# Kernel optimization log

Measured on AMD Instinct MI355X. Metric: run time of the kernel, lower is better.

Reference implementation:

```python
import jax, jax.numpy as jnp
import numpy as np

B, L = 16, 2048
D_MODEL, D_INNER, D_STATE, DT_RANK, D_CONV = 128, 256, 16, 8, 4
N_LAYERS, N_CLASSES = 4, 5
EPS = 1e-5


def setup_inputs() -> dict:
    key = jax.random.key(0)
    ks = jax.random.split(key, 12)
    rn = lambda k, shape, s=0.02: jax.random.normal(k, shape, jnp.float32) * s
    A_log = jnp.log(jnp.arange(1, D_STATE + 1, dtype=jnp.float32))  # S4D-real init
    return dict(
        x=jax.random.normal(ks[0], (B, L, 12), jnp.float32),
        enc_w=rn(ks[1], (D_MODEL, 12), 0.1),
        enc_b=jnp.zeros((D_MODEL,), jnp.float32),
        norm_w=jnp.ones((N_LAYERS, D_MODEL), jnp.float32),
        in_proj_w=rn(ks[2], (N_LAYERS, 2 * D_INNER, D_MODEL)),
        conv_w=rn(ks[3], (N_LAYERS, D_INNER, D_CONV), 0.1),
        conv_b=jnp.zeros((N_LAYERS, D_INNER), jnp.float32),
        x_proj_w=rn(ks[4], (N_LAYERS, DT_RANK + 2 * D_STATE, D_INNER)),
        dt_proj_w=rn(ks[5], (N_LAYERS, D_INNER, DT_RANK), 0.1),
        dt_proj_b=rn(ks[6], (N_LAYERS, D_INNER), 0.1),
        A_log=jnp.broadcast_to(A_log, (N_LAYERS, D_INNER, D_STATE)) + 0.0,
        Dp=jnp.ones((N_LAYERS, D_INNER), jnp.float32),
        out_proj_w=rn(ks[7], (N_LAYERS, D_MODEL, D_INNER)),
        norm_f_w=jnp.ones((D_MODEL,), jnp.float32),
        cls_w=rn(ks[8], (N_CLASSES, D_MODEL), 0.05),
        cls_b=jnp.zeros((N_CLASSES,), jnp.float32),
    )


def rmsnorm(x, w):
    return x * jax.lax.rsqrt(jnp.mean(x * x, axis=-1, keepdims=True) + EPS) * w


def causal_depthwise_conv(x, w, b):
    # x: [b, l, di]; w: [di, k]; causal (left) padding, groups=di
    xc = x.transpose(0, 2, 1)  # [b, di, l]
    y = jax.lax.conv_general_dilated(
        xc, w[:, None, :], window_strides=(1,), padding=[(D_CONV - 1, 0)],
        dimension_numbers=("NCH", "OIH", "NCH"), feature_group_count=D_INNER)
    return (y + b[None, :, None]).transpose(0, 2, 1)


def selective_scan(u, delta, A, Bm, Cm, Dv):
    # u, delta: [b,l,di]; A: [di,n]; Bm, Cm: [b,l,n]; Dv: [di]
    dA = jnp.exp(jnp.einsum("bld,dn->bldn", delta, A))          # [b,l,di,n]
    dBu = jnp.einsum("bld,bln,bld->bldn", delta, Bm, u)          # [b,l,di,n]

    def step(h, inp):
        dA_t, dBu_t, C_t = inp
        h = dA_t * h + dBu_t                                     # [b,di,n]
        y = jnp.einsum("bdn,bn->bd", h, C_t)
        return h, y

    h0 = jnp.zeros((u.shape[0], u.shape[2], A.shape[1]), u.dtype)
    xs = (dA.transpose(1, 0, 2, 3), dBu.transpose(1, 0, 2, 3), Cm.transpose(1, 0, 2))
    _, ys = jax.lax.scan(step, h0, xs)
    return ys.transpose(1, 0, 2) + u * Dv


def mamba_block(x, in_w, cw, cb, xp_w, dt_w, dt_b, A_log_i, D_i, out_w):
    xz = jnp.einsum("bld,ed->ble", x, in_w)                      # [b,l,2*di]
    xm, z = xz[..., :D_INNER], xz[..., D_INNER:]
    xm = jax.nn.silu(causal_depthwise_conv(xm, cw, cb))
    x_dbl = jnp.einsum("bld,ed->ble", xm, xp_w)                  # [b,l,dt_rank+2n]
    dt = x_dbl[..., :DT_RANK]
    Bm = x_dbl[..., DT_RANK:DT_RANK + D_STATE]
    Cm = x_dbl[..., DT_RANK + D_STATE:]
    delta = jax.nn.softplus(jnp.einsum("blr,dr->bld", dt, dt_w) + dt_b)
    A = -jnp.exp(A_log_i)
    y = selective_scan(xm, delta, A, Bm, Cm, D_i)
    y = y * jax.nn.silu(z)
    return jnp.einsum("bld,ed->ble", y, out_w)


def reference(x, enc_w, enc_b, norm_w, in_proj_w, conv_w, conv_b, x_proj_w,
              dt_proj_w, dt_proj_b, A_log, Dp, out_proj_w, norm_f_w, cls_w, cls_b):
    h = jnp.einsum("blc,dc->bld", x, enc_w) + enc_b               # conv1d k=1 encoder
    for i in range(N_LAYERS):
        h = mamba_block(rmsnorm(h, norm_w[i]), in_proj_w[i], conv_w[i], conv_b[i],
                        x_proj_w[i], dt_proj_w[i], dt_proj_b[i], A_log[i], Dp[i],
                        out_proj_w[i]) + h
    h = rmsnorm(h, norm_f_w)
    pooled = jnp.mean(h, axis=1)                                  # AdaptiveAvgPool1d(1)
    return pooled @ cls_w.T + cls_b                               # [B, n_classes]
```

## Files before the change

### kernel.cpp

```cpp
#include <hip/hip_runtime.h>
#include <hip/hip_bf16.h>
#include <cstddef>

#define BB 16
#define LL 2048
#define DM 128
#define DI 256
#define DS 16
#define MP (BB*LL)
#define NSEG 64
#define SEGLEN (LL/NSEG)
#define YSTR 264
#define XSTR 40

typedef __attribute__((ext_vector_type(8))) short bf16x8;
typedef __attribute__((ext_vector_type(4))) short bf16x4s;
typedef __attribute__((ext_vector_type(8))) unsigned int ux8;
typedef __attribute__((ext_vector_type(4))) float f32x4;
typedef __hip_bfloat16 bf16;
typedef unsigned int uint;

__device__ inline void bf16split(float x, bf16& h, bf16& l) {
  h = __float2bfloat16(x);
  l = __float2bfloat16(x - __bfloat162float(h));
}
__device__ inline float bf2f(bf16 v) { return __bfloat162float(v); }
__device__ inline void split_bits2(float x, short& hs, short& ls) {
  bf16 hb = __float2bfloat16(x);
  bf16 lb = __float2bfloat16(x - __bfloat162float(hb));
  hs = *(short*)&hb;
  ls = *(short*)&lb;
}
__device__ inline short bfbits(float x) {
  bf16 b = __float2bfloat16(x);
  return *(short*)&b;
}
__device__ inline float sigm(float x) {
  return __builtin_amdgcn_rcpf(1.f + __expf(-x));
}
__device__ inline uint pk2(short h, short l) {
  return (uint)(unsigned short)h | ((uint)(unsigned short)l << 16);
}
__device__ inline uint pack_hl(float x) {
  short hs, ls; split_bits2(x, hs, ls);
  return pk2(hs, ls);
}
__device__ inline float unpack_hl(uint w) {
  return __uint_as_float(w << 16) + __uint_as_float(w & 0xffff0000u);
}

__global__ __launch_bounds__(256, 2) void gemm_inproj_conv(
    const bf16* __restrict__ Ah, const bf16* __restrict__ Al,
    const bf16* __restrict__ Wh, const bf16* __restrict__ Wl,
    const bf16* __restrict__ Xh, const bf16* __restrict__ Xl,
    const float* __restrict__ cw, const float* __restrict__ cb,
    uint* __restrict__ zs_pk, uint* __restrict__ u_pk,
    float* __restrict__ C) {
  __shared__ uint  xmb[35 * 260];
  __shared__ short ubh[32 * 264];
  __shared__ short ubl[32 * 264];
  __shared__ float scw[DI * 4 + DI];
  int tid = threadIdx.x;
  {
    float4 w4 = *(const float4*)(cw + tid * 4);
    *(float4*)(scw + tid * 4) = w4;
    scw[DI * 4 + tid] = cb[tid];
  }
  int wave = tid >> 6, lane = tid & 63;
  int r16 = lane & 15, quad = lane >> 4;
  int m0 = blockIdx.x * 32;

  size_t arow[3];
#pragma unroll
  for (int rt = 0; rt < 3; rt++) {
    int rg = m0 - 16 + rt * 16 + r16;
    if (rg < 0) rg = 0;
    arow[rt] = (size_t)rg * DM + quad * 8;
  }
  size_t browx[4], browz[4];
#pragma unroll
  for (int ct = 0; ct < 4; ct++) {
    browx[ct] = (size_t)(wave * 64 + ct * 16 + r16) * DM + quad * 8;
    browz[ct] = (size_t)(256 + wave * 64 + ct * 16 + r16) * DM + quad * 8;
  }
  f32x4 accx[3][4] = {};
  f32x4 accz[2][4] = {};
#pragma unroll
  for (int kk = 0; kk < 4; kk++) {
    int ko = kk * 32;
    bf16x8 ah[3], al[3], bxh[4], bxl[4], bzh[4], bzl[4];
#pragma unroll
    for (int rt = 0; rt < 3; rt++) {
      ah[rt] = *(const bf16x8*)(Ah + arow[rt] + ko);
      al[rt] = *(const bf16x8*)(Al + arow[rt] + ko);
    }
#pragma unroll
    for (int ct = 0; ct < 4; ct++) {
      bxh[ct] = *(const bf16x8*)(Wh + browx[ct] + ko);
      bxl[ct] = *(const bf16x8*)(Wl + browx[ct] + ko);
      bzh[ct] = *(const bf16x8*)(Wh + browz[ct] + ko);
      bzl[ct] = *(const bf16x8*)(Wl + browz[ct] + ko);
    }
#pragma unroll
    for (int rt = 0; rt < 3; rt++)
#pragma unroll
      for (int ct = 0; ct < 4; ct++) {
        accx[rt][ct] = __builtin_amdgcn_mfma_f32_16x16x32_bf16(ah[rt], bxh[ct], accx[rt][ct], 0, 0, 0);
        accx[rt][ct] = __builtin_amdgcn_mfma_f32_16x16x32_bf16(ah[rt], bxl[ct], accx[rt][ct], 0, 0, 0);
        accx[rt][ct] = __builtin_amdgcn_mfma_f32_16x16x32_bf16(al[rt], bxh[ct], accx[rt][ct], 0, 0, 0);
      }
#pragma unroll
    for (int rz = 0; rz < 2; rz++)
#pragma unroll
      for (int ct = 0; ct < 4; ct++) {
        accz[rz][ct] = __builtin_amdgcn_mfma_f32_16x16x32_bf16(ah[rz + 1], bzh[ct], accz[rz][ct], 0, 0, 0);
        accz[rz][ct] = __builtin_amdgcn_mfma_f32_16x16x32_bf16(ah[rz + 1], bzl[ct], accz[rz][ct], 0, 0, 0);
        accz[rz][ct] = __builtin_amdgcn_mfma_f32_16x16x32_bf16(al[rz + 1], bzh[ct], accz[rz][ct], 0, 0, 0);
      }
  }
#pragma unroll
  for (int rz = 0; rz < 2; rz++)
#pragma unroll
    for (int ct = 0; ct < 4; ct++)
#pragma unroll
      for (int r = 0; r < 4; r++) {
        int row = m0 + rz * 16 + quad * 4 + r;
        int col = wave * 64 + ct * 16 + r16;
        float v = accz[rz][ct][r];
        v *= sigm(v);
        zs_pk[(size_t)row * DI + col] = pack_hl(v);
      }
#pragma unroll
  for (int rt = 0; rt < 3; rt++)
#pragma unroll
    for (int ct = 0; ct < 4; ct++)
#pragma unroll
      for (int r = 0; r < 4; r++) {
        int lidx = rt * 16 + quad * 4 + r - 13;
        if (lidx >= 0)
          xmb[lidx * 260 + wave * 64 + ct * 16 + r16] = pack_hl(accx[rt][ct][r]);
      }
  __syncthreads();

  {
    int d = tid;
    float w0 = scw[d * 4], w1 = scw[d * 4 + 1], w2 = scw[d * 4 + 2], w3 = scw[d * 4 + 3];
    float bias = scw[DI * 4 + d];
    float xa = unpack_hl(xmb[0 * 260 + d]);
    float xb = unpack_hl(xmb[1 * 260 + d]);
    float xc = unpack_hl(xmb[2 * 260 + d]);
    int lbase = m0 & (LL - 1);
#pragma unroll 4
    for (int t = 0; t < 32; t++) {
      float xd = unpack_hl(xmb[(t + 3) * 260 + d]);
      int l = lbase + t;
      float x0 = xa * ((l >= 3) ? 1.f : 0.f);
      float x1 = xb * ((l >= 2) ? 1.f : 0.f);
      float x2 = xc * ((l >= 1) ? 1.f : 0.f);
      float c0 = bias + w0 * x0 + w1 * x1 + w2 * x2 + w3 * xd;
      float u = c0 * sigm(c0);
      short hs, ls; split_bits2(u, hs, ls);
      u_pk[(size_t)(m0 + t) * DI + d] = pk2(hs, ls);
      ubh[t * 264 + d] = hs;
      ubl[t * 264 + d] = ls;
      xa = xb; xb = xc; xc = xd;
    }
  }
  __syncthreads();

  {
    int rt0 = (wave == 3) ? 1 : 0;
    int ct0 = (wave == 0) ? 0 : (wave == 1) ? 1 : (wave == 2) ? 2 : 0;
#pragma unroll 1
    for (int tt = 0; tt < 2; tt++) {
      int rt, ct;
      if (tt == 0) { rt = rt0; ct = ct0; }
      else { if (wave >= 2) break; rt = 1; ct = wave + 1; }
      f32x4 a2 = {};
#pragma unroll
      for (int kk = 0; kk < 8; kk++) {
        int k0 = quad * 8 + kk * 32;
        bf16x8 ahh = *(const bf16x8*)(ubh + (rt * 16 + r16) * 264 + k0);
        bf16x8 alo = *(const bf16x8*)(ubl + (rt * 16 + r16) * 264 + k0);
        size_t br = (size_t)(ct * 16 + r16) * DI + quad * 8 + kk * 32;
        bf16x8 bhh = *(const bf16x8*)(Xh + br);
        bf16x8 blo = *(const bf16x8*)(Xl + br);
        a2 = __builtin_amdgcn_mfma_f32_16x16x32_bf16(ahh, bhh, a2, 0, 0, 0);
        a2 = __builtin_amdgcn_mfma_f32_16x16x32_bf16(ahh, blo, a2, 0, 0, 0);
        a2 = __builtin_amdgcn_mfma_f32_16x16x32_bf16(alo, bhh, a2, 0, 0, 0);
      }
#pragma unroll
      for (int r = 0; r < 4; r++)
        C[(size_t)(m0 + rt * 16 + quad * 4 + r) * 64 + ct * 16 + r16] = a2[r];
    }
  }
}

__global__ __launch_bounds__(256) void encoder_kernel(const float* __restrict__ x,
    const float* __restrict__ ew, const float* __restrict__ eb,
    float* __restrict__ h) {
  int idx = blockIdx.x * 256 + threadIdx.x;
  int d = idx & 127, m = idx >> 7;
  float acc = eb[d];
#pragma unroll
  for (int c = 0; c < 12; c++) acc += x[m * 12 + c] * ew[d * 12 + c];
  h[idx] = acc;
}

__global__ void split_w(const float* __restrict__ src, bf16* __restrict__ hi,
                        bf16* __restrict__ lo, int n) {
  int i = blockIdx.x * 256 + threadIdx.x;
  if (i < n) bf16split(src[i], hi[i], lo[i]);
}

__global__ void split_w_pad(const float* __restrict__ src, bf16* __restrict__ hi,
                            bf16* __restrict__ lo) {
  int i = blockIdx.x * 256 + threadIdx.x;
  int l = i >> 14, rem = i & 16383, r = rem >> 8, k = rem & 255;
  float v = (r < 40) ? src[l * 10240 + r * 256 + k] : 0.f;
  bf16split(v, hi[i], lo[i]);
}

__global__ __launch_bounds__(256) void rmsnorm_kernel(const float* __restrict__ x,
    const float* __restrict__ w, bf16* __restrict__ oh, bf16* __restrict__ ol) {
  int lane = threadIdx.x & 63;
  int pos = blockIdx.x * 4 + (threadIdx.x >> 6);
  const float* row = x + (size_t)pos * DM;
  float v0 = row[lane], v1 = row[lane + 64];
  float ss = v0 * v0 + v1 * v1;
#pragma unroll
  for (int off = 1; off < 64; off <<= 1) ss += __shfl_xor(ss, off);
  float sc = rsqrtf(ss * (1.f / DM) + 1e-5f);
  float a = v0 * sc * w[lane], b = v1 * sc * w[lane + 64];
  size_t o = (size_t)pos * DM;
  bf16split(a, oh[o + lane], ol[o + lane]);
  bf16split(b, oh[o + lane + 64], ol[o + lane + 64]);
}

__device__ inline float softplus_f(float a) {
  float r = __logf(1.f + __expf(a));
  return a > 15.f ? a : r;
}

__device__ inline void make_powers(float r, float* rp) {
  rp[0] = r;
#pragma unroll
  for (int n = 1; n < 16; n++) {
    int a = (n + 1) >> 1, b = (n + 1) - a;
    rp[n] = rp[a - 1] * rp[b - 1];
  }
}

__device__ inline bool a_is_integer(const float* A_log, int d) {
  bool ok = true;
#pragma unroll
  for (int n = 0; n < DS; n++) {
    float Ad = -__expf(A_log[d * DS + n]);
    ok = ok && (fabsf(Ad + (float)(n + 1)) < 1e-3f);
  }
  return ok;
}

__device__ inline void load_sx(float* sx, const float* xdbl, size_t rbase, int tid) {
#pragma unroll
  for (int j = 0; j < 2; j++) {
    int idx = j * 256 + tid;
    if (idx < 320) {
      int row = idx / 10, c = idx % 10;
      *(float4*)(sx + row * XSTR + c * 4) = *(const float4*)(xdbl + rbase + row * 64 + c * 4);
    }
  }
}

template<bool FAST>
__device__ inline void scan1_body(int s, int b, int d, const float* sx,
    const uint* __restrict__ u_pk,
    const float* __restrict__ dtw, const float* __restrict__ dtb,
    const float* __restrict__ A_log,
    float* __restrict__ sega, float* __restrict__ segh) {
  float wdt[8];
#pragma unroll
  for (int j = 0; j < 8; j++) wdt[j] = dtw[d * 8 + j];
  float bdt = dtb[d];
  float h[DS];
#pragma unroll
  for (int n = 0; n < DS; n++) h[n] = 0.f;
  float R = 1.f;
  float ap[DS];
  if (!FAST) {
#pragma unroll
    for (int n = 0; n < DS; n++) ap[n] = 1.f;
  }
  size_t base = (size_t)b * LL + (size_t)s * SEGLEN;
  const uint* up = u_pk + base * DI + d;
  uint ub = *up;
#pragma unroll 4
  for (int t = 0; t < SEGLEN; t++) {
    up += DI;
    uint ub_next = *up;
    const float* xr = sx + t * XSTR;
    float dt = bdt;
#pragma unroll
    for (int j = 0; j < 8; j++) dt += xr[j] * wdt[j];
    float dl = softplus_f(dt);
    float u = unpack_hl(ub);
    float du = dl * u;
    if (FAST) {
      float rp[DS];
      make_powers(__expf(-dl), rp);
      R *= rp[0];
#pragma unroll
      for (int n = 0; n < DS; n++) h[n] = fmaf(rp[n], h[n], du * xr[8 + n]);
    } else {
#pragma unroll
      for (int n = 0; n < DS; n++) {
        float dA = __expf(dl * (-__expf(A_log[d * DS + n])));
        h[n] = fmaf(dA, h[n], du * xr[8 + n]);
        ap[n] *= dA;
      }
    }
    ub = ub_next;
  }
  if (FAST) make_powers(R, ap);
  size_t o = ((size_t)s * 4096 + b * 256 + d) * DS;
#pragma unroll
  for (int j = 0; j < 4; j++) {
    *(float4*)(sega + o + 4 * j) = make_float4(ap[4*j], ap[4*j+1], ap[4*j+2], ap[4*j+3]);
    *(float4*)(segh + o + 4 * j) = make_float4(h[4*j], h[4*j+1], h[4*j+2], h[4*j+3]);
  }
}

__global__ __launch_bounds__(256, 6) void scan_phase1(
    const uint* __restrict__ u_pk, const float* __restrict__ xdbl,
    const float* __restrict__ dtw, const float* __restrict__ dtb,
    const float* __restrict__ A_log,
    float* __restrict__ sega, float* __restrict__ segh) {
  __shared__ float sx[SEGLEN * XSTR];
  int s = blockIdx.x, b = blockIdx.y, d = threadIdx.x;
  size_t rbase = ((size_t)b * LL + (size_t)s * SEGLEN) * 64;
  load_sx(sx, xdbl, rbase, d);
  __syncthreads();
  if (a_is_integer(A_log, d))
    scan1_body<true>(s, b, d, sx, u_pk, dtw, dtb, A_log, sega, segh);
  else
    scan1_body<false>(s, b, d, sx, u_pk, dtw, dtb, A_log, sega, segh);
}

__global__ __launch_bounds__(256) void scan_combine(float* __restrict__ sega,
    const float* __restrict__ segh) {
  int g = blockIdx.x * 256 + threadIdx.x;
  size_t off = (size_t)(g >> 2) * 16 + (g & 3) * 4;
  float4 h0 = make_float4(0.f, 0.f, 0.f, 0.f);
  for (int s = 0; s < NSEG; s++) {
    size_t q = (size_t)s * 65536 + off;
    float4 a = *(float4*)(sega + q);
    float4 hh = *(float4*)(segh + q);
    *(float4*)(sega + q) = h0;
    h0.x = a.x * h0.x + hh.x;
    h0.y = a.y * h0.y + hh.y;
    h0.z = a.z * h0.z + hh.z;
    h0.w = a.w * h0.w + hh.w;
  }
}

template<bool FAST>
__device__ inline void scan2_to_lds(int s, int b, int d, const float* sx,
    const uint* __restrict__ u_pk, const uint* __restrict__ zs_pk,
    const float* __restrict__ dtw, const float* __restrict__ dtb,
    const float* __restrict__ A_log, const float* __restrict__ Dp,
    const float* __restrict__ sega, short* __restrict__ ybuf) {
  float wdt[8];
#pragma unroll
  for (int j = 0; j < 8; j++) wdt[j] = dtw[d * 8 + j];
  float bdt = dtb[d];
  float h[DS];
  size_t o = ((size_t)s * 4096 + b * 256 + d) * DS;
#pragma unroll
  for (int n = 0; n < DS; n++) h[n] = sega[o + n];
  float Dd = Dp[d];
  size_t base = (size_t)b * LL + (size_t)s * SEGLEN;
  const uint* up = u_pk + base * DI + d;
  const uint* zp = zs_pk + base * DI + d;
  uint ub = *up, zb = *zp;
#pragma unroll 4
  for (int t = 0; t < SEGLEN; t++) {
    up += DI; zp += DI;
    uint ub_next = *up;
    uint zb_next = *zp;
    const float* xr = sx + t * XSTR;
    float dt = bdt;
#pragma unroll
    for (int j = 0; j < 8; j++) dt += xr[j] * wdt[j];
    float dl = softplus_f(dt);
    float u = unpack_hl(ub);
    float du = dl * u;
    float acc = 0.f;
    if (FAST) {
      float rp[DS];
      make_powers(__expf(-dl), rp);
#pragma unroll
      for (int n = 0; n < DS; n++) {
        h[n] = fmaf(rp[n], h[n], du * xr[8 + n]);
        acc = fmaf(h[n], xr[24 + n], acc);
      }
    } else {
#pragma unroll
      for (int n = 0; n < DS; n++) {
        float dA = __expf(dl * (-__expf(A_log[d * DS + n])));
        h[n] = fmaf(dA, h[n], du * xr[8 + n]);
        acc = fmaf(h[n], xr[24 + n], acc);
      }
    }
    float zs = unpack_hl(zb);
    float yv = (acc + u * Dd) * zs;
    ybuf[t * YSTR + d] = bfbits(yv);
    ub = ub_next; zb = zb_next;
  }
}

__global__ __launch_bounds__(256, 6) void scan2_outproj(
    const uint* __restrict__ u_pk, const uint* __restrict__ zs_pk,
    const float* __restrict__ xdbl, const float* __restrict__ dtw,
    const float* __restrict__ dtb, const float* __restrict__ A_log,
    const float* __restrict__ Dp, const float* __restrict__ sega,
    const bf16* __restrict__ Wh, const bf16* __restrict__ Wl,
    float* __restrict__ hbuf, const float* __restrict__ nw,
    float* __restrict__ of, bf16* __restrict__ oh, bf16* __restrict__ ol) {
  __shared__ float sx[SEGLEN * XSTR];
  __shared__ short ybuf[32 * YSTR];
  int s = blockIdx.x, b = blockIdx.y;
  int tid = threadIdx.x, d = tid;
  size_t rbase = ((size_t)b * LL + (size_t)s * SEGLEN) * 64;
  load_sx(sx, xdbl, rbase, tid);
  __syncthreads();
  if (a_is_integer(A_log, d))
    scan2_to_lds<true>(s, b, d, sx, u_pk, zs_pk, dtw, dtb, A_log, Dp, sega, ybuf);
  else
    scan2_to_lds<false>(s, b, d, sx, u_pk, zs_pk, dtw, dtb, A_log, Dp, sega, ybuf);
  __syncthreads();
  int wave = tid >> 6, lane = tid & 63;
  int r16 = lane & 15, quad = lane >> 4;
  int n0 = wave * 32;
  size_t brow[2];
#pragma unroll
  for (int j = 0; j < 2; j++)
    brow[j] = (size_t)(n0 + j * 16 + r16) * DI + quad * 8;
  f32x4 acc[2][2] = {};
#pragma unroll
  for (int kk = 0; kk < 8; kk++) {
    int k0 = quad * 8 + kk * 32;
    bf16x8 ah[2], bh[2], bl[2];
#pragma unroll
    for (int i = 0; i < 2; i++)
      ah[i] = *(const bf16x8*)(ybuf + (i * 16 + r16) * YSTR + k0);
#pragma unroll
    for (int j = 0; j < 2; j++) {
      bh[j] = *(const bf16x8*)(Wh + brow[j] + kk * 32);
      bl[j] = *(const bf16x8*)(Wl + brow[j] + kk * 32);
    }
#pragma unroll
    for (int i = 0; i < 2; i++)
#pragma unroll
      for (int j = 0; j < 2; j++) {
        acc[i][j] = __builtin_amdgcn_mfma_f32_16x16x32_bf16(ah[i], bh[j], acc[i][j], 0, 0, 0);
        acc[i][j] = __builtin_amdgcn_mfma_f32_16x16x32_bf16(ah[i], bl[j], acc[i][j], 0, 0, 0);
      }
  }
  __syncthreads();
  float* tile = (float*)ybuf;
#pragma unroll
  for (int i = 0; i < 2; i++)
#pragma unroll
    for (int j = 0; j < 2; j++)
#pragma unroll
      for (int r = 0; r < 4; r++) {
        int rl = i * 16 + quad * 4 + r;
        int col = n0 + j * 16 + r16;
        tile[rl * 132 + col] = acc[i][j][r];
      }
  __syncthreads();
  size_t mbase = (size_t)b * LL + (size_t)s * SEGLEN;
#pragma unroll
  for (int it = 0; it < 4; it++) {
    int idx = it * 256 + tid;
    int row = idx >> 5, c4 = idx & 31;
    size_t g = (mbase + row) * DM + c4 * 4;
    float4 hv = *(float4*)(hbuf + g);
    const float* tp = tile + row * 132 + c4 * 4;
    float4 v = make_float4(tp[0] + hv.x, tp[1] + hv.y, tp[2] + hv.z, tp[3] + hv.w);
    *(float4*)(hbuf + g) = v;
    float ss = v.x * v.x + v.y * v.y + v.z * v.z + v.w * v.w;
    ss += __shfl_xor(ss, 1);
    ss += __shfl_xor(ss, 2);
    ss += __shfl_xor(ss, 4);
    ss += __shfl_xor(ss, 8);
    ss += __shfl_xor(ss, 16);
    float sc = rsqrtf(ss * (1.f / DM) + 1e-5f);
    float4 w4 = *(const float4*)(nw + c4 * 4);
    float n0v = v.x * sc * w4.x, n1v = v.y * sc * w4.y;
    float n2v = v.z * sc * w4.z, n3v = v.w * sc * w4.w;
    if (of) *(float4*)(of + g) = make_float4(n0v, n1v, n2v, n3v);
    short h0s, l0s, h1s, l1s, h2s, l2s, h3s, l3s;
    split_bits2(n0v, h0s, l0s); split_bits2(n1v, h1s, l1s);
    split_bits2(n2v, h2s, l2s); split_bits2(n3v, h3s, l3s);
    bf16x4s hb, lb;
    hb[0] = h0s; hb[1] = h1s; hb[2] = h2s; hb[3] = h3s;
    lb[0] = l0s; lb[1] = l1s; lb[2] = l2s; lb[3] = l3s;
    *(bf16x4s*)(oh + g) = hb;
    *(bf16x4s*)(ol + g) = lb;
  }
}

__global__ __launch_bounds__(256) void pool_partial(const float* __restrict__ fn,
    float* __restrict__ partial) {
  __shared__ float red[256];
  int b = blockIdx.x, c = blockIdx.y;
  int tid = threadIdx.x;
  int d = tid & 127, rp_ = tid >> 7;
  float s = 0.f;
  size_t base = (size_t)b * LL + c * 256;
  for (int i = 0; i < 128; i++) {
    int row = i * 2 + rp_;
    s += fn[(base + row) * DM + d];
  }
  red[tid] = s;
  __syncthreads();
  if (tid < 128) partial[((size_t)b * 8 + c) * 128 + tid] = red[tid] + red[tid + 128];
}

__global__ void pool_reduce(const float* __restrict__ partial,
    float* __restrict__ pooled) {
  int idx = blockIdx.x * 256 + threadIdx.x;
  int b = idx >> 7, d = idx & 127;
  float s = 0.f;
#pragma unroll
  for (int c = 0; c < 8; c++) s += partial[((size_t)b * 8 + c) * 128 + d];
  pooled[idx] = s * (1.f / LL);
}

__global__ void cls_kernel(const float* __restrict__ pooled,
    const float* __restrict__ cw, const float* __restrict__ cb,
    float* __restrict__ out) {
  int t = threadIdx.x;
  if (t < 80) {
    int b = t / 5, c = t % 5;
    float acc = cb[c];
    for (int d = 0; d < DM; d++) acc += pooled[b * DM + d] * cw[c * DM + d];
    out[t] = acc;
  }
}

extern "C" void kernel_launch(void* const* d_in, const int* in_sizes, int n_in,
                              void* d_out, int out_size, void* d_ws, size_t ws_size,
                              hipStream_t stream) {
  const float* x         = (const float*)d_in[0];
  const float* enc_w     = (const float*)d_in[1];
  const float* enc_b     = (const float*)d_in[2];
  const float* norm_w    = (const float*)d_in[3];
  const float* in_proj_w = (const float*)d_in[4];
  const float* conv_w    = (const float*)d_in[5];
  const float* conv_b    = (const float*)d_in[6];
  const float* x_proj_w  = (const float*)d_in[7];
  const float* dt_proj_w = (const float*)d_in[8];
  const float* dt_proj_b = (const float*)d_in[9];
  const float* A_log     = (const float*)d_in[10];
  const float* Dp        = (const float*)d_in[11];
  const float* out_proj_w= (const float*)d_in[12];
  const float* norm_f_w  = (const float*)d_in[13];
  const float* cls_w     = (const float*)d_in[14];
  const float* cls_b     = (const float*)d_in[15];
  float* out = (float*)d_out;

  float* ws = (float*)d_ws;
  float* h       = ws;
  float* xdbl    = ws + 4194304;
  float* sega    = ws + 6291456;
  float* segh    = ws + 10485760;
  uint*  zs_pk   = (uint*)(ws + 14680064);
  uint*  u_pk    = (uint*)(ws + 23068672);
  uint*  xm_pk   = (uint*)(ws + 31457280);
  float* partial = ws + 39845888;
  float* pooled  = ws + 39862272;
  bf16* u0     = (bf16*)(ws + 39864320);
  bf16* xn_hi  = u0;
  bf16* xn_lo  = u0 + 4194304;
  bf16* wip_hi = u0 + 8388608;
  bf16* wip_lo = wip_hi + 262144;
  bf16* wxp_hi = wip_lo + 262144;
  bf16* wxp_lo = wxp_hi + 65536;
  bf16* wop_hi = wxp_lo + 65536;
  bf16* wop_lo = wop_hi + 131072;
  float* fnorm = (float*)xm_pk;

  split_w<<<1024, 256, 0, stream>>>(in_proj_w, wip_hi, wip_lo, 262144);
  split_w_pad<<<256, 256, 0, stream>>>(x_proj_w, wxp_hi, wxp_lo);
  split_w<<<512, 256, 0, stream>>>(out_proj_w, wop_hi, wop_lo, 131072);

  encoder_kernel<<<MP * DM / 256, 256, 0, stream>>>(x, enc_w, enc_b, h);
  rmsnorm_kernel<<<MP / 4, 256, 0, stream>>>(h, norm_w, xn_hi, xn_lo);

  for (int i = 0; i < 4; i++) {
    gemm_inproj_conv<<<MP / 32, 256, 0, stream>>>(xn_hi, xn_lo,
        wip_hi + i * 65536, wip_lo + i * 65536,
        wxp_hi + i * 16384, wxp_lo + i * 16384,
        conv_w + i * DI * 4, conv_b + i * DI,
        zs_pk, u_pk, xdbl);
    scan_phase1<<<dim3(NSEG, BB), 256, 0, stream>>>(u_pk, xdbl,
        dt_proj_w + i * 2048, dt_proj_b + i * DI, A_log + i * DI * DS, sega, segh);
    scan_combine<<<64, 256, 0, stream>>>(sega, segh);
    scan2_outproj<<<dim3(NSEG, BB), 256, 0, stream>>>(u_pk, zs_pk, xdbl,
        dt_proj_w + i * 2048, dt_proj_b + i * DI, A_log + i * DI * DS,
        Dp + i * DI, sega, wop_hi + i * 32768, wop_lo + i * 32768, h,
        (i < 3) ? norm_w + (i + 1) * DM : norm_f_w,
        (i < 3) ? nullptr : fnorm, xn_hi, xn_lo);
  }

  pool_partial<<<dim3(BB, 8), 256, 0, stream>>>(fnorm, partial);
  pool_reduce<<<8, 256, 0, stream>>>(partial, pooled);
  cls_kernel<<<1, 128, 0, stream>>>(pooled, cls_w, cls_b, out);
}
```

Baseline: 701.0 us.

## Fuse scan phase-1 segment reduction into in-projection/conv GEMM kernel

```diff
diff --git a/kernel.cpp b/kernel.cpp
--- a/kernel.cpp
+++ b/kernel.cpp
@@ -12,6 +12,7 @@
 #define SEGLEN (LL/NSEG)
 #define YSTR 264
 #define XSTR 40
+#define SXS 48
 
 typedef __attribute__((ext_vector_type(8))) short bf16x8;
 typedef __attribute__((ext_vector_type(4))) short bf16x4s;
@@ -49,13 +50,92 @@
   return __uint_as_float(w << 16) + __uint_as_float(w & 0xffff0000u);
 }
 
+__device__ inline float softplus_f(float a) {
+  float r = __logf(1.f + __expf(a));
+  return a > 15.f ? a : r;
+}
+
+__device__ inline void make_powers(float r, float* rp) {
+  rp[0] = r;
+#pragma unroll
+  for (int n = 1; n < 16; n++) {
+    int a = (n + 1) >> 1, b = (n + 1) - a;
+    rp[n] = rp[a - 1] * rp[b - 1];
+  }
+}
+
+__device__ inline bool a_is_integer(const float* A_log, int d) {
+  bool ok = true;
+#pragma unroll
+  for (int n = 0; n < DS; n++) {
+    float Ad = -__expf(A_log[d * DS + n]);
+    ok = ok && (fabsf(Ad + (float)(n + 1)) < 1e-3f);
+  }
+  return ok;
+}
+
+template<bool FAST>
+__device__ inline void scan1_lds(int s, int b, int d,
+    const float* sx, const short* ubh, const short* ubl,
+    const float* __restrict__ dtw, const float* __restrict__ dtb,
+    const float* __restrict__ A_log,
+    float* __restrict__ sega, float* __restrict__ segh) {
+  float wdt[8];
+#pragma unroll
+  for (int j = 0; j < 8; j++) wdt[j] = dtw[d * 8 + j];
+  float bdt = dtb[d];
+  float h[DS];
+#pragma unroll
+  for (int n = 0; n < DS; n++) h[n] = 0.f;
+  float R = 1.f;
+  float ap[DS];
+  if (!FAST) {
+#pragma unroll
+    for (int n = 0; n < DS; n++) ap[n] = 1.f;
+  }
+#pragma unroll 4
+  for (int t = 0; t < SEGLEN; t++) {
+    const float* xr = sx + t * SXS;
+    float dt = bdt;
+#pragma unroll
+    for (int j = 0; j < 8; j++) dt += xr[j] * wdt[j];
+    float dl = softplus_f(dt);
+    float u = unpack_hl(pk2(ubh[t * 264 + d], ubl[t * 264 + d]));
+    float du = dl * u;
+    if (FAST) {
+      float rp[DS];
+      make_powers(__expf(-dl), rp);
+      R *= rp[0];
+#pragma unroll
+      for (int n = 0; n < DS; n++) h[n] = fmaf(rp[n], h[n], du * xr[8 + n]);
+    } else {
+#pragma unroll
+      for (int n = 0; n < DS; n++) {
+        float dA = __expf(dl * (-__expf(A_log[d * DS + n])));
+        h[n] = fmaf(dA, h[n], du * xr[8 + n]);
+        ap[n] *= dA;
+      }
+    }
+  }
+  if (FAST) make_powers(R, ap);
+  size_t o = ((size_t)s * 4096 + b * 256 + d) * DS;
+#pragma unroll
+  for (int j = 0; j < 4; j++) {
+    *(float4*)(sega + o + 4 * j) = make_float4(ap[4*j], ap[4*j+1], ap[4*j+2], ap[4*j+3]);
+    *(float4*)(segh + o + 4 * j) = make_float4(h[4*j], h[4*j+1], h[4*j+2], h[4*j+3]);
+  }
+}
+
 __global__ __launch_bounds__(256, 2) void gemm_inproj_conv(
     const bf16* __restrict__ Ah, const bf16* __restrict__ Al,
     const bf16* __restrict__ Wh, const bf16* __restrict__ Wl,
     const bf16* __restrict__ Xh, const bf16* __restrict__ Xl,
     const float* __restrict__ cw, const float* __restrict__ cb,
+    const float* __restrict__ dtw, const float* __restrict__ dtb,
+    const float* __restrict__ A_log,
     uint* __restrict__ zs_pk, uint* __restrict__ u_pk,
-    float* __restrict__ C) {
+    float* __restrict__ C,
+    float* __restrict__ sega, float* __restrict__ segh) {
   __shared__ uint  xmb[35 * 260];
   __shared__ short ubh[32 * 264];
   __shared__ short ubl[32 * 264];
@@ -168,6 +248,7 @@
   }
   __syncthreads();
 
+  float* sx = (float*)xmb;
   {
     int rt0 = (wave == 3) ? 1 : 0;
     int ct0 = (wave == 0) ? 0 : (wave == 1) ? 1 : (wave == 2) ? 2 : 0;
@@ -190,9 +271,22 @@
         a2 = __builtin_amdgcn_mfma_f32_16x16x32_bf16(alo, bhh, a2, 0, 0, 0);
       }
 #pragma unroll
-      for (int r = 0; r < 4; r++)
-        C[(size_t)(m0 + rt * 16 + quad * 4 + r) * 64 + ct * 16 + r16] = a2[r];
-    }
+      for (int r = 0; r < 4; r++) {
+        int row = rt * 16 + quad * 4 + r;
+        int col = ct * 16 + r16;
+        C[(size_t)(m0 + row) * 64 + col] = a2[r];
+        sx[row * SXS + col] = a2[r];
+      }
+    }
+  }
+  __syncthreads();
+
+  {
+    int b = blockIdx.x >> 6, s = blockIdx.x & 63, d = tid;
+    if (a_is_integer(A_log, d))
+      scan1_lds<true>(s, b, d, sx, ubh, ubl, dtw, dtb, A_log, sega, segh);
+    else
+      scan1_lds<false>(s, b, d, sx, ubh, ubl, dtw, dtb, A_log, sega, segh);
   }
 }
 
@@ -237,30 +331,6 @@
   bf16split(b, oh[o + lane + 64], ol[o + lane + 64]);
 }
 
-__device__ inline float softplus_f(float a) {
-  float r = __logf(1.f + __expf(a));
-  return a > 15.f ? a : r;
-}
-
-__device__ inline void make_powers(float r, float* rp) {
-  rp[0] = r;
-#pragma unroll
-  for (int n = 1; n < 16; n++) {
-    int a = (n + 1) >> 1, b = (n + 1) - a;
-    rp[n] = rp[a - 1] * rp[b - 1];
-  }
-}
-
-__device__ inline bool a_is_integer(const float* A_log, int d) {
-  bool ok = true;
-#pragma unroll
-  for (int n = 0; n < DS; n++) {
-    float Ad = -__expf(A_log[d * DS + n]);
-    ok = ok && (fabsf(Ad + (float)(n + 1)) < 1e-3f);
-  }
-  return ok;
-}
-
 __device__ inline void load_sx(float* sx, const float* xdbl, size_t rbase, int tid) {
 #pragma unroll
   for (int j = 0; j < 2; j++) {
@@ -270,80 +340,6 @@
       *(float4*)(sx + row * XSTR + c * 4) = *(const float4*)(xdbl + rbase + row * 64 + c * 4);
     }
   }
-}
-
-template<bool FAST>
-__device__ inline void scan1_body(int s, int b, int d, const float* sx,
-    const uint* __restrict__ u_pk,
-    const float* __restrict__ dtw, const float* __restrict__ dtb,
-    const float* __restrict__ A_log,
-    float* __restrict__ sega, float* __restrict__ segh) {
-  float wdt[8];
-#pragma unroll
-  for (int j = 0; j < 8; j++) wdt[j] = dtw[d * 8 + j];
-  float bdt = dtb[d];
-  float h[DS];
-#pragma unroll
-  for (int n = 0; n < DS; n++) h[n] = 0.f;
-  float R = 1.f;
-  float ap[DS];
-  if (!FAST) {
-#pragma unroll
-    for (int n = 0; n < DS; n++) ap[n] = 1.f;
-  }
-  size_t base = (size_t)b * LL + (size_t)s * SEGLEN;
-  const uint* up = u_pk + base * DI + d;
-  uint ub = *up;
-#pragma unroll 4
-  for (int t = 0; t < SEGLEN; t++) {
-    up += DI;
-    uint ub_next = *up;
-    const float* xr = sx + t * XSTR;
-    float dt = bdt;
-#pragma unroll
-    for (int j = 0; j < 8; j++) dt += xr[j] * wdt[j];
-    float dl = softplus_f(dt);
-    float u = unpack_hl(ub);
-    float du = dl * u;
-    if (FAST) {
-      float rp[DS];
-      make_powers(__expf(-dl), rp);
-      R *= rp[0];
-#pragma unroll
-      for (int n = 0; n < DS; n++) h[n] = fmaf(rp[n], h[n], du * xr[8 + n]);
-    } else {
-#pragma unroll
-      for (int n = 0; n < DS; n++) {
-        float dA = __expf(dl * (-__expf(A_log[d * DS + n])));
-        h[n] = fmaf(dA, h[n], du * xr[8 + n]);
-        ap[n] *= dA;
-      }
-    }
-    ub = ub_next;
-  }
-  if (FAST) make_powers(R, ap);
-  size_t o = ((size_t)s * 4096 + b * 256 + d) * DS;
-#pragma unroll
-  for (int j = 0; j < 4; j++) {
-    *(float4*)(sega + o + 4 * j) = make_float4(ap[4*j], ap[4*j+1], ap[4*j+2], ap[4*j+3]);
-    *(float4*)(segh + o + 4 * j) = make_float4(h[4*j], h[4*j+1], h[4*j+2], h[4*j+3]);
-  }
-}
-
-__global__ __launch_bounds__(256, 6) void scan_phase1(
-    const uint* __restrict__ u_pk, const float* __restrict__ xdbl,
-    const float* __restrict__ dtw, const float* __restrict__ dtb,
-    const float* __restrict__ A_log,
-    float* __restrict__ sega, float* __restrict__ segh) {
-  __shared__ float sx[SEGLEN * XSTR];
-  int s = blockIdx.x, b = blockIdx.y, d = threadIdx.x;
-  size_t rbase = ((size_t)b * LL + (size_t)s * SEGLEN) * 64;
-  load_sx(sx, xdbl, rbase, d);
-  __syncthreads();
-  if (a_is_integer(A_log, d))
-    scan1_body<true>(s, b, d, sx, u_pk, dtw, dtb, A_log, sega, segh);
-  else
-    scan1_body<false>(s, b, d, sx, u_pk, dtw, dtb, A_log, sega, segh);
 }
 
 __global__ __launch_bounds__(256) void scan_combine(float* __restrict__ sega,
@@ -604,9 +600,8 @@
         wip_hi + i * 65536, wip_lo + i * 65536,
         wxp_hi + i * 16384, wxp_lo + i * 16384,
         conv_w + i * DI * 4, conv_b + i * DI,
-        zs_pk, u_pk, xdbl);
-    scan_phase1<<<dim3(NSEG, BB), 256, 0, stream>>>(u_pk, xdbl,
-        dt_proj_w + i * 2048, dt_proj_b + i * DI, A_log + i * DI * DS, sega, segh);
+        dt_proj_w + i * 2048, dt_proj_b + i * DI, A_log + i * DI * DS,
+        zs_pk, u_pk, xdbl, sega, segh);
     scan_combine<<<64, 256, 0, stream>>>(sega, segh);
     scan2_outproj<<<dim3(NSEG, BB), 256, 0, stream>>>(u_pk, zs_pk, xdbl,
         dt_proj_w + i * 2048, dt_proj_b + i * DI, A_log + i * DI * DS,
```

Result: faster. 661.8 us (-5.6%).
